# Performance work log

Measured on AMD Instinct MI355X. Metric: run time of the kernel, lower is better.

The kernel has to match this reference:

```python
import jax, jax.numpy as jnp
import numpy as np

B, L, H, HEADS = 4, 2048, 512, 8
D = H // HEADS  # 64


def setup_inputs() -> dict:
    key = jax.random.key(0)
    ks = jax.random.split(key, 13)
    s = 0.02
    return {
        "q_in": jax.random.normal(ks[0], (B, L, H), jnp.float32),
        "k_in": jax.random.normal(ks[1], (B, L, H), jnp.float32),
        "v_in": jax.random.normal(ks[2], (B, L, H), jnp.float32),
        "Wq_w": jax.random.normal(ks[3], (H, H), jnp.float32) * s,
        "Wq_b": jax.random.normal(ks[4], (H,), jnp.float32) * s,
        "Wk_w": jax.random.normal(ks[5], (H, H), jnp.float32) * s,
        "Wk_b": jax.random.normal(ks[6], (H,), jnp.float32) * s,
        "Wv_w": jax.random.normal(ks[7], (H, H), jnp.float32) * s,
        "Wv_b": jax.random.normal(ks[8], (H,), jnp.float32) * s,
        "Wo_w": jax.random.normal(ks[9], (H, H), jnp.float32) * s,
        "Wo_b": jax.random.normal(ks[10], (H,), jnp.float32) * s,
        "Wp_w": jax.random.normal(ks[11], (2 * L - 1, D), jnp.float32) * s,
        "Wp_b": jax.random.normal(ks[12], (2 * L - 1,), jnp.float32) * s,
    }


def _skew(p):
    # p: (b, h, l, 2l-1) -> relative-position bias (b, h, l, l) via pad/flatten/reshape skew trick
    b, h, l, _ = p.shape
    p = jnp.pad(p, ((0, 0), (0, 0), (0, 0), (0, 1)))          # (b,h,l,2l)
    p = p.reshape(b, h, 2 * l * l)
    p = jnp.pad(p, ((0, 0), (0, 0), (0, l - 1)))               # (b,h,(l+1)(2l-1))
    p = p.reshape(b, h, l + 1, 2 * l - 1)
    return p[:, :, :-1, -l:]                                   # (b,h,l,l)


def reference(q_in, k_in, v_in, Wq_w, Wq_b, Wk_w, Wk_b, Wv_w, Wv_b, Wo_w, Wo_b, Wp_w, Wp_b):
    b, l, hid = q_in.shape
    q = q_in @ Wq_w.T + Wq_b
    k = k_in @ Wk_w.T + Wk_b
    v = v_in @ Wv_w.T + Wv_b
    # (b, l, h*d) -> (b, h, l, d)
    to_heads = lambda x: x.reshape(b, l, HEADS, D).transpose(0, 2, 1, 3)
    q, k, v = to_heads(q), to_heads(k), to_heads(v)
    q = q / jnp.sqrt(jnp.asarray(D, q.dtype))  # scaling applied BEFORE posenc, as in original
    scores = jnp.einsum('bhid,bhjd->bhij', q, k)
    pos = _skew(q @ Wp_w.T + Wp_b)             # posenc linear applied to scaled q
    scores = scores + pos
    attn = jax.nn.softmax(scores, axis=-1)     # (b,h,l,l)
    # Original torch.einsum('b h l l, b h l d -> b h l d') takes the DIAGONAL of attn
    diag = jnp.diagonal(attn, axis1=-2, axis2=-1)  # (b,h,l)
    out = diag[..., None] * v                       # (b,h,l,d)
    out = out.transpose(0, 2, 1, 3).reshape(b, l, hid)
    return out @ Wo_w.T + Wo_b
```

## Files before the change

kernel.cpp:

```cpp
#include <hip/hip_runtime.h>
#include <cstdint>


typedef unsigned short u16;
typedef __bf16 bf16x8 __attribute__((ext_vector_type(8)));
typedef __bf16 bf16x2 __attribute__((ext_vector_type(2)));
typedef float  f32x16 __attribute__((ext_vector_type(16)));
typedef uint32_t __attribute__((address_space(1))) as1_u32;
typedef uint32_t __attribute__((address_space(3))) as3_u32;

__device__ __forceinline__ u16 f2bf(float f) {
  __bf16 h = (__bf16)f;
  return __builtin_bit_cast(u16, h);
}
__device__ __forceinline__ uint32_t pkbf(float a, float b) {
  bf16x2 v; v[0] = (__bf16)a; v[1] = (__bf16)b;
  return __builtin_bit_cast(uint32_t, v);
}
__device__ __forceinline__ float bf2f(u16 u) {
  return __uint_as_float(((uint32_t)u) << 16);
}
__device__ __forceinline__ float exp2v(float x) {
  float r;
  asm("v_exp_f32 %0, %1" : "=v"(r) : "v"(x));
  return r;
}
__device__ __forceinline__ void gl_lds16(const void* g, void* l) {
  __builtin_amdgcn_global_load_lds((const as1_u32*)g, (as3_u32*)l, 16, 0, 0);
}

__global__ __launch_bounds__(256) void prep_kernel(
    const float* __restrict__ qin, const float* __restrict__ kin, const float* __restrict__ vin,
    const float* __restrict__ wq,  const float* __restrict__ wk,  const float* __restrict__ wv,
    const float* __restrict__ wo,  const float* __restrict__ wp,
    u16* __restrict__ xq, u16* __restrict__ xk, u16* __restrict__ xv,
    u16* __restrict__ bwq, u16* __restrict__ bwk, u16* __restrict__ bwv,
    u16* __restrict__ bwo, u16* __restrict__ bwp) {
  long u = (long)blockIdx.x * 256 + threadIdx.x;
  const float* src; u16* dst; long off; float qs = 1.0f;
  if      (u < 524288L)  { src = qin; dst = xq;  off = u; }
  else if (u < 1048576L) { src = kin; dst = xk;  off = u - 524288L; }
  else if (u < 1572864L) { src = vin; dst = xv;  off = u - 1048576L; }
  else if (u < 1605632L) { src = wq;  dst = bwq; off = u - 1572864L; qs = 0.18033688f; }
  else if (u < 1638400L) { src = wk;  dst = bwk; off = u - 1605632L; }
  else if (u < 1671168L) { src = wv;  dst = bwv; off = u - 1638400L; }
  else if (u < 1703936L) { src = wo;  dst = bwo; off = u - 1671168L; }
  else if (u < 1736696L) { src = wp;  dst = bwp; off = u - 1703936L; }
  else {
    long o = (u - 1736696L) * 8 + 262080L;
    uint4 z = {0u, 0u, 0u, 0u};
    *(uint4*)(bwp + o) = z;
    return;
  }
  const float4* s4 = (const float4*)(src + off * 8);
  float4 a = s4[0], b = s4[1];
  uint32_t p0 = pkbf(a.x * qs, a.y * qs);
  uint32_t p1 = pkbf(a.z * qs, a.w * qs);
  uint32_t p2 = pkbf(b.x * qs, b.y * qs);
  uint32_t p3 = pkbf(b.z * qs, b.w * qs);
  uint4 o = {p0, p1, p2, p3};
  *(uint4*)(dst + off * 8) = o;
}

__device__ __forceinline__ void gemm64_core(
    const u16* __restrict__ A, const u16* __restrict__ W, int m0, int n0,
    u16* Al, u16* Bl, int tid, f32x16& acc) {
  const int lane = tid & 63, w = tid >> 6;
  const int wi = w >> 1, wj = w & 1;
  const int l31 = lane & 31, lh = lane >> 5;
  const int r = tid >> 2, ch = tid & 3;
  const int gch = ch ^ ((r >> 1) & 3);
  for (int kb = 0; kb < 16; ++kb) {
    gl_lds16(A + (long)(m0 + r) * 512 + kb * 32 + gch * 8, (char*)Al + w * 64 * 16);
    gl_lds16(W + (long)(n0 + r) * 512 + kb * 32 + gch * 8, (char*)Bl + w * 64 * 16);
    __syncthreads();
    bf16x8 af[2], bfr[2];
#pragma unroll
    for (int ks = 0; ks < 2; ++ks) {
      int c2 = 2 * ks + lh;
      int rA = 32 * wi + l31;
      int rB = 32 * wj + l31;
      af[ks]  = *(const bf16x8*)((char*)Al + (rA * 4 + (c2 ^ ((rA >> 1) & 3))) * 16);
      bfr[ks] = *(const bf16x8*)((char*)Bl + (rB * 4 + (c2 ^ ((rB >> 1) & 3))) * 16);
    }
#pragma unroll
    for (int ks = 0; ks < 2; ++ks)
      acc = __builtin_amdgcn_mfma_f32_32x32x16_bf16(af[ks], bfr[ks], acc, 0, 0, 0);
    __syncthreads();
  }
}

__global__ __launch_bounds__(256, 4) void gemm_bt(
    const u16* __restrict__ A, const u16* __restrict__ W, const float* __restrict__ bias,
    float* __restrict__ ofp) {
  __shared__ u16 Al[64 * 32];
  __shared__ u16 Bl[64 * 32];
  const int tid = threadIdx.x;
  const int lane = tid & 63, w = tid >> 6;
  const int wi = w >> 1, wj = w & 1;
  const int l31 = lane & 31, lh = lane >> 5;
  const int u = (blockIdx.x & 7) * 128 + (blockIdx.x >> 3);
  const int m0 = (u >> 3) * 64, n0 = (u & 7) * 64;

  float bv = bias[n0 + 32 * wj + l31];
  f32x16 acc;
#pragma unroll
  for (int rr = 0; rr < 16; ++rr) acc[rr] = bv;

  gemm64_core(A, W, m0, n0, Al, Bl, tid, acc);

  int n = n0 + 32 * wj + l31;
#pragma unroll
  for (int rr = 0; rr < 16; ++rr) {
    int row = m0 + 32 * wi + (rr & 3) + 8 * (rr >> 2) + 4 * lh;
    ofp[(long)row * 512 + n] = acc[rr];
  }
}

__global__ __launch_bounds__(256, 4) void qkv_gemm(
    const u16* __restrict__ xq, const u16* __restrict__ xk, const u16* __restrict__ xv,
    const u16* __restrict__ wqp, const u16* __restrict__ wkp, const u16* __restrict__ wvp,
    const float* __restrict__ bq, const float* __restrict__ bk, const float* __restrict__ bv,
    u16* __restrict__ oq, u16* __restrict__ ok, u16* __restrict__ ov) {
  __shared__ u16 Al[64 * 32];
  __shared__ u16 Bl[64 * 32];
  const int mat = blockIdx.x >> 10;
  const int t = blockIdx.x & 1023;
  const u16* A = (mat == 0) ? xq : (mat == 1) ? xk : xv;
  const u16* W = (mat == 0) ? wqp : (mat == 1) ? wkp : wvp;
  const float* bias = (mat == 0) ? bq : (mat == 1) ? bk : bv;
  u16* obf = (mat == 0) ? oq : (mat == 1) ? ok : ov;
  const float bsc = (mat == 0) ? 0.18033688f : 1.0f;

  const int tid = threadIdx.x;
  const int lane = tid & 63, w = tid >> 6;
  const int wi = w >> 1, wj = w & 1;
  const int l31 = lane & 31, lh = lane >> 5;
  const int u = (t & 7) * 128 + (t >> 3);
  const int m0 = (u >> 3) * 64, n0 = (u & 7) * 64;

  float bvv = bias[n0 + 32 * wj + l31] * bsc;
  f32x16 acc;
#pragma unroll
  for (int rr = 0; rr < 16; ++rr) acc[rr] = bvv;

  gemm64_core(A, W, m0, n0, Al, Bl, tid, acc);

  int n = n0 + 32 * wj + l31;
  int h = n >> 6, d = n & 63;
#pragma unroll
  for (int rr = 0; rr < 16; ++rr) {
    int row = m0 + 32 * wi + (rr & 3) + 8 * (rr >> 2) + 4 * lh;
    int b = row >> 11, l = row & 2047;
    obf[(((long)(b * 8 + h)) * 2048 + l) * 64 + d] = f2bf(acc[rr]);
  }
}

#define PCOMP(RING, G, AQ0, AQ1, AQ2, AQ3, B0, B1, B2, B3, BV)                   \
  do {                                                                           \
    f32x16 accP;                                                                 \
    _Pragma("unroll")                                                            \
    for (int r = 0; r < 16; ++r) accP[r] = (BV);                                 \
    accP = __builtin_amdgcn_mfma_f32_32x32x16_bf16(AQ0, B0, accP, 0, 0, 0);      \
    accP = __builtin_amdgcn_mfma_f32_32x32x16_bf16(AQ1, B1, accP, 0, 0, 0);      \
    accP = __builtin_amdgcn_mfma_f32_32x32x16_bf16(AQ2, B2, accP, 0, 0, 0);      \
    accP = __builtin_amdgcn_mfma_f32_32x32x16_bf16(AQ3, B3, accP, 0, 0, 0);      \
    int bw_ = 32 * (G) + l31 + 4 * lh;                                           \
    _Pragma("unroll")                                                            \
    for (int r = 0; r < 16; ++r) {                                               \
      const int lrr = (r & 3) + 8 * (r >> 2);                                    \
      int uu = (bw_ + lrr) & 127;                                                \
      (RING)[uu * 36 + lrr + 4 * lh] = f2bf(accP[r]);                            \
    }                                                                            \
  } while (0)

#define GATH(RING, T, ACC)                                                       \
  do {                                                                           \
    int u_ = (31 + l31 + 32 * (T)) & 127;                                        \
    const u16* p_ = (RING) + u_ * 36 + 4 * lh;                                   \
    uint2 g0 = *(const uint2*)(p_);                                              \
    uint2 g1 = *(const uint2*)(p_ + 8);                                          \
    uint2 g2 = *(const uint2*)(p_ + 16);                                         \
    uint2 g3 = *(const uint2*)(p_ + 24);                                         \
    ACC[0]  = __uint_as_float(g0.x << 16); ACC[1]  = __uint_as_float(g0.x & 0xffff0000u); \
    ACC[2]  = __uint_as_float(g0.y << 16); ACC[3]  = __uint_as_float(g0.y & 0xffff0000u); \
    ACC[4]  = __uint_as_float(g1.x << 16); ACC[5]  = __uint_as_float(g1.x & 0xffff0000u); \
    ACC[6]  = __uint_as_float(g1.y << 16); ACC[7]  = __uint_as_float(g1.y & 0xffff0000u); \
    ACC[8]  = __uint_as_float(g2.x << 16); ACC[9]  = __uint_as_float(g2.x & 0xffff0000u); \
    ACC[10] = __uint_as_float(g2.y << 16); ACC[11] = __uint_as_float(g2.y & 0xffff0000u); \
    ACC[12] = __uint_as_float(g3.x << 16); ACC[13] = __uint_as_float(g3.x & 0xffff0000u); \
    ACC[14] = __uint_as_float(g3.y << 16); ACC[15] = __uint_as_float(g3.y & 0xffff0000u); \
  } while (0)

#define ATTN_STEP(T, DO_P)                                                       \
  do {                                                                           \
    const int t_ = (T);                                                          \
    const u16* kp_ = kb + (long)(c0 + 32 * t_ + l31) * 64 + lh * 8;              \
    bf16x8 kf0 = *(const bf16x8*)(kp_);                                          \
    bf16x8 kf1 = *(const bf16x8*)(kp_ + 16);                                     \
    bf16x8 kf2 = *(const bf16x8*)(kp_ + 32);                                     \
    bf16x8 kf3 = *(const bf16x8*)(kp_ + 48);                                     \
    {                                                                            \
      f32x16 accS;                                                               \
      GATH(ringA, t_, accS);                                                     \
      accS = __builtin_amdgcn_mfma_f32_32x32x16_bf16(aqA0, kf0, accS, 0, 0, 0);  \
      accS = __builtin_amdgcn_mfma_f32_32x32x16_bf16(aqA1, kf1, accS, 0, 0, 0);  \
      accS = __builtin_amdgcn_mfma_f32_32x32x16_bf16(aqA2, kf2, accS, 0, 0, 0);  \
      accS = __builtin_amdgcn_mfma_f32_32x32x16_bf16(aqA3, kf3, accS, 0, 0, 0);  \
      if (diagw && t_ == tdA) {                                                  \
        _Pragma("unroll")                                                        \
        for (int r = 0; r < 16; ++r) {                                           \
          const int lrr = (r & 3) + 8 * (r >> 2);                                \
          if (l31 == lrr + 4 * lh) sdiag[lrr + 4 * lh] = accS[r];                \
        }                                                                        \
      }                                                                          \
      _Pragma("unroll")                                                          \
      for (int r = 0; r < 16; ++r) rsum[r] += exp2v(accS[r]);                    \
    }                                                                            \
    {                                                                            \
      f32x16 accS;                                                               \
      GATH(ringB, t_, accS);                                                     \
      accS = __builtin_amdgcn_mfma_f32_32x32x16_bf16(aqB0, kf0, accS, 0, 0, 0);  \
      accS = __builtin_amdgcn_mfma_f32_32x32x16_bf16(aqB1, kf1, accS, 0, 0, 0);  \
      accS = __builtin_amdgcn_mfma_f32_32x32x16_bf16(aqB2, kf2, accS, 0, 0, 0);  \
      accS = __builtin_amdgcn_mfma_f32_32x32x16_bf16(aqB3, kf3, accS, 0, 0, 0);  \
      if (diagw && t_ == tdA + 1) {                                              \
        _Pragma("unroll")                                                        \
        for (int r = 0; r < 16; ++r) {                                           \
          const int lrr = (r & 3) + 8 * (r >> 2);                                \
          if (l31 == lrr + 4 * lh) sdiag[32 + lrr + 4 * lh] = accS[r];           \
        }                                                                        \
      }                                                                          \
      _Pragma("unroll")                                                          \
      for (int r = 0; r < 16; ++r) rsum[16 + r] += exp2v(accS[r]);               \
    }                                                                            \
    if (DO_P) {                                                                  \
      int wr_ = wbA + 32 * (t_ + 2) + l31;                                       \
      const u16* bp_ = wpw + (long)wr_ * 64 + lh * 8;                            \
      bf16x8 nb0 = *(const bf16x8*)(bp_);                                        \
      bf16x8 nb1 = *(const bf16x8*)(bp_ + 16);                                   \
      bf16x8 nb2 = *(const bf16x8*)(bp_ + 32);                                   \
      bf16x8 nb3 = *(const bf16x8*)(bp_ + 48);                                   \
      float nbv = wpb[wr_ > 4094 ? 4094 : wr_] * 1.44269504f;                    \
      PCOMP(ringB, t_ + 2, aqB0, aqB1, aqB2, aqB3, cb0, cb1, cb2, cb3, cbv);     \
      PCOMP(ringA, t_ + 2, aqA0, aqA1, aqA2, aqA3, nb0, nb1, nb2, nb3, nbv);     \
      cb0 = nb0; cb1 = nb1; cb2 = nb2; cb3 = nb3; cbv = nbv;                     \
    }                                                                            \
  } while (0)

__global__ __launch_bounds__(256, 2) void attn_kernel(
    const u16* __restrict__ qw, const u16* __restrict__ kw, const u16* __restrict__ vw,
    const u16* __restrict__ wpw, const float* __restrict__ wpb, u16* __restrict__ outp) {
  __shared__ u16 Pl[8 * 128 * 36];
  __shared__ float sdiag[64];
  __shared__ float rssum[64 * 4];
  __shared__ float attw[64];

  const int tid = threadIdx.x, lane = tid & 63, w = tid >> 6;
  const int sbi = blockIdx.x;
  const int x = sbi & 7, g = sbi >> 3;
  const int bh = x + 8 * (g >> 5);
  const int it = g & 31;
  const int i0 = it * 64;
  const u16* qb = qw + (long)bh * 2048 * 64;
  const u16* kb = kw + (long)bh * 2048 * 64;
  const u16* vb = vw + (long)bh * 2048 * 64;

  const int l31 = lane & 31, lh = lane >> 5;
  const int c0 = w << 9;
  const int wbA = 2016 + c0 - i0;
  const bool diagw = (w == (it >> 3));
  const int tdA = 2 * (it & 7);

  u16* ringA = Pl + w * 9216;
  u16* ringB = ringA + 4608;

  bf16x8 aqA0, aqA1, aqA2, aqA3, aqB0, aqB1, aqB2, aqB3;
  {
    const u16* pA = qb + (long)(i0 + l31) * 64 + lh * 8;
    aqA0 = *(const bf16x8*)(pA);
    aqA1 = *(const bf16x8*)(pA + 16);
    aqA2 = *(const bf16x8*)(pA + 32);
    aqA3 = *(const bf16x8*)(pA + 48);
    const u16* pB = pA + 32 * 64;
    aqB0 = *(const bf16x8*)(pB);
    aqB1 = *(const bf16x8*)(pB + 16);
    aqB2 = *(const bf16x8*)(pB + 32);
    aqB3 = *(const bf16x8*)(pB + 48);
  }

  float rsum[32];
#pragma unroll
  for (int r = 0; r < 32; ++r) rsum[r] = 0.f;

  bf16x8 cb0, cb1, cb2, cb3;
  float cbv;

  {
    int wr = wbA - 32 + l31;
    const u16* bp = wpw + (long)wr * 64 + lh * 8;
    bf16x8 f0 = *(const bf16x8*)(bp), f1 = *(const bf16x8*)(bp + 16);
    bf16x8 f2 = *(const bf16x8*)(bp + 32), f3 = *(const bf16x8*)(bp + 48);
    float fv = wpb[wr > 4094 ? 4094 : wr] * 1.44269504f;
    PCOMP(ringB, 0, aqB0, aqB1, aqB2, aqB3, f0, f1, f2, f3, fv);
  }
  {
    int wr = wbA + l31;
    const u16* bp = wpw + (long)wr * 64 + lh * 8;
    bf16x8 f0 = *(const bf16x8*)(bp), f1 = *(const bf16x8*)(bp + 16);
    bf16x8 f2 = *(const bf16x8*)(bp + 32), f3 = *(const bf16x8*)(bp + 48);
    float fv = wpb[wr > 4094 ? 4094 : wr] * 1.44269504f;
    PCOMP(ringA, 0, aqA0, aqA1, aqA2, aqA3, f0, f1, f2, f3, fv);
    PCOMP(ringB, 1, aqB0, aqB1, aqB2, aqB3, f0, f1, f2, f3, fv);
  }
  {
    int wr = wbA + 32 + l31;
    const u16* bp = wpw + (long)wr * 64 + lh * 8;
    cb0 = *(const bf16x8*)(bp); cb1 = *(const bf16x8*)(bp + 16);
    cb2 = *(const bf16x8*)(bp + 32); cb3 = *(const bf16x8*)(bp + 48);
    cbv = wpb[wr > 4094 ? 4094 : wr] * 1.44269504f;
    PCOMP(ringA, 1, aqA0, aqA1, aqA2, aqA3, cb0, cb1, cb2, cb3, cbv);
  }

  for (int t = 0; t < 15; ++t) {
    ATTN_STEP(t, true);
  }
  ATTN_STEP(15, false);

#pragma unroll
  for (int r = 0; r < 32; ++r) {
    float v = rsum[r];
    v += __shfl_xor(v, 1);
    v += __shfl_xor(v, 2);
    v += __shfl_xor(v, 4);
    v += __shfl_xor(v, 8);
    v += __shfl_xor(v, 16);
    rsum[r] = v;
  }
  if (l31 == 0) {
#pragma unroll
    for (int r = 0; r < 16; ++r) {
      int lr = (r & 3) + 8 * (r >> 2) + 4 * lh;
      rssum[lr * 4 + w] = rsum[r];
      rssum[(32 + lr) * 4 + w] = rsum[16 + r];
    }
  }
  __syncthreads();
  if (tid < 64) {
    float S = rssum[tid * 4] + rssum[tid * 4 + 1] + rssum[tid * 4 + 2] + rssum[tid * 4 + 3];
    attw[tid] = exp2v(sdiag[tid]) / S;
  }
  __syncthreads();
  {
    int r = tid >> 2, dd = (tid & 3) * 16;
    float a = attw[r];
    int b = bh >> 3, h = bh & 7;
    const u16* vp = vb + (long)(i0 + r) * 64 + dd;
    u16* op = outp + ((long)(b * 2048 + i0 + r)) * 512 + h * 64 + dd;
    uint4 v0 = *(const uint4*)vp;
    uint4 v1 = *(const uint4*)(vp + 8);
    uint32_t vin[8] = {v0.x, v0.y, v0.z, v0.w, v1.x, v1.y, v1.z, v1.w};
    uint32_t vout[8];
#pragma unroll
    for (int e = 0; e < 8; ++e) {
      float lo = bf2f((u16)(vin[e] & 0xffffu)) * a;
      float hi = bf2f((u16)(vin[e] >> 16)) * a;
      vout[e] = pkbf(lo, hi);
    }
    uint4 o0 = {vout[0], vout[1], vout[2], vout[3]};
    uint4 o1 = {vout[4], vout[5], vout[6], vout[7]};
    *(uint4*)op = o0;
    *(uint4*)(op + 8) = o1;
  }
}

extern "C" void kernel_launch(void* const* d_in, const int* in_sizes, int n_in,
                              void* d_out, int out_size, void* d_ws, size_t ws_size,
                              hipStream_t stream) {
  (void)in_sizes; (void)n_in; (void)out_size; (void)ws_size;
  const float* q_in = (const float*)d_in[0];
  const float* k_in = (const float*)d_in[1];
  const float* v_in = (const float*)d_in[2];
  const float* Wq_w = (const float*)d_in[3];
  const float* Wq_b = (const float*)d_in[4];
  const float* Wk_w = (const float*)d_in[5];
  const float* Wk_b = (const float*)d_in[6];
  const float* Wv_w = (const float*)d_in[7];
  const float* Wv_b = (const float*)d_in[8];
  const float* Wo_w = (const float*)d_in[9];
  const float* Wo_b = (const float*)d_in[10];
  const float* Wp_w = (const float*)d_in[11];
  const float* Wp_b = (const float*)d_in[12];

  char* ws = (char*)d_ws;
  u16* xq    = (u16*)(ws + 0);
  u16* xk    = (u16*)(ws + 8388608);
  u16* xv    = (u16*)(ws + 16777216);
  u16* wq    = (u16*)(ws + 25165824);
  u16* wk    = (u16*)(ws + 25690112);
  u16* wv    = (u16*)(ws + 26214400);
  u16* wo    = (u16*)(ws + 26738688);
  u16* wp    = (u16*)(ws + 27262976);
  u16* q_ws  = (u16*)(ws + 27787264);
  u16* k_ws  = (u16*)(ws + 36175872);
  u16* v_ws  = (u16*)(ws + 44564480);
  u16* opre  = (u16*)(ws + 52953088);

  prep_kernel<<<6784, 256, 0, stream>>>(q_in, k_in, v_in, Wq_w, Wk_w, Wv_w, Wo_w, Wp_w,
                                        xq, xk, xv, wq, wk, wv, wo, wp);
  qkv_gemm<<<3072, 256, 0, stream>>>(xq, xk, xv, wq, wk, wv, Wq_b, Wk_b, Wv_b,
                                     q_ws, k_ws, v_ws);
  attn_kernel<<<1024, 256, 0, stream>>>(q_ws, k_ws, v_ws, wp, Wp_b, opre);
  gemm_bt<<<1024, 256, 0, stream>>>(opre, wo, Wo_b, (float*)d_out);
}
```

Baseline: 224.2 us.

## Software-pipeline K and posenc loads, prefetch ring gathers, and pad LDS rows

The attention loop now double-buffers K fragments and Wp rows in registers. The loads for step t+1 and t+2 are issued before the current step's MFMAs, and the next step's LDS gathers are done at the end of each step, so global and LDS latency overlap with compute. The LDS ring stride goes from 36 to 38 u16 per row and the gathers become 32-bit loads, which aims to reduce bank conflicts. The cost is higher register pressure under launch_bounds(256,2), which could cause spills, plus slightly more shared memory.

```diff
diff --git a/kernel.cpp b/kernel.cpp
--- a/kernel.cpp
+++ b/kernel.cpp
@@ -156,6 +156,26 @@
   }
 }
 
+#define LOADK(T, K0, K1, K2, K3)                                                 \
+  do {                                                                           \
+    const u16* kp_ = kb + (long)(c0 + 32 * (T) + l31) * 64 + lh * 8;             \
+    K0 = *(const bf16x8*)(kp_);                                                  \
+    K1 = *(const bf16x8*)(kp_ + 16);                                             \
+    K2 = *(const bf16x8*)(kp_ + 32);                                             \
+    K3 = *(const bf16x8*)(kp_ + 48);                                             \
+  } while (0)
+
+#define LOADNB(M, N0, N1, N2, N3, NV)                                            \
+  do {                                                                           \
+    int wr_ = wbA + 32 * (M) + l31;                                              \
+    const u16* bp_ = wpw + (long)wr_ * 64 + lh * 8;                              \
+    N0 = *(const bf16x8*)(bp_);                                                  \
+    N1 = *(const bf16x8*)(bp_ + 16);                                             \
+    N2 = *(const bf16x8*)(bp_ + 32);                                             \
+    N3 = *(const bf16x8*)(bp_ + 48);                                             \
+    NV = wpb[wr_ > 4094 ? 4094 : wr_] * 1.44269504f;                             \
+  } while (0)
+
 #define PCOMP(RING, G, AQ0, AQ1, AQ2, AQ3, B0, B1, B2, B3, BV)                   \
   do {                                                                           \
     f32x16 accP;                                                                 \
@@ -170,88 +190,71 @@
     for (int r = 0; r < 16; ++r) {                                               \
       const int lrr = (r & 3) + 8 * (r >> 2);                                    \
       int uu = (bw_ + lrr) & 127;                                                \
-      (RING)[uu * 36 + lrr + 4 * lh] = f2bf(accP[r]);                            \
+      (RING)[uu * 38 + lrr + 4 * lh] = f2bf(accP[r]);                            \
     }                                                                            \
   } while (0)
 
 #define GATH(RING, T, ACC)                                                       \
   do {                                                                           \
     int u_ = (31 + l31 + 32 * (T)) & 127;                                        \
-    const u16* p_ = (RING) + u_ * 36 + 4 * lh;                                   \
-    uint2 g0 = *(const uint2*)(p_);                                              \
-    uint2 g1 = *(const uint2*)(p_ + 8);                                          \
-    uint2 g2 = *(const uint2*)(p_ + 16);                                         \
-    uint2 g3 = *(const uint2*)(p_ + 24);                                         \
-    ACC[0]  = __uint_as_float(g0.x << 16); ACC[1]  = __uint_as_float(g0.x & 0xffff0000u); \
-    ACC[2]  = __uint_as_float(g0.y << 16); ACC[3]  = __uint_as_float(g0.y & 0xffff0000u); \
-    ACC[4]  = __uint_as_float(g1.x << 16); ACC[5]  = __uint_as_float(g1.x & 0xffff0000u); \
-    ACC[6]  = __uint_as_float(g1.y << 16); ACC[7]  = __uint_as_float(g1.y & 0xffff0000u); \
-    ACC[8]  = __uint_as_float(g2.x << 16); ACC[9]  = __uint_as_float(g2.x & 0xffff0000u); \
-    ACC[10] = __uint_as_float(g2.y << 16); ACC[11] = __uint_as_float(g2.y & 0xffff0000u); \
-    ACC[12] = __uint_as_float(g3.x << 16); ACC[13] = __uint_as_float(g3.x & 0xffff0000u); \
-    ACC[14] = __uint_as_float(g3.y << 16); ACC[15] = __uint_as_float(g3.y & 0xffff0000u); \
+    const uint32_t* p_ = (const uint32_t*)((RING) + u_ * 38 + 4 * lh);           \
+    uint32_t g0 = p_[0], g1 = p_[1], g2 = p_[4],  g3 = p_[5];                    \
+    uint32_t g4 = p_[8], g5 = p_[9], g6 = p_[12], g7 = p_[13];                   \
+    ACC[0]  = __uint_as_float(g0 << 16); ACC[1]  = __uint_as_float(g0 & 0xffff0000u); \
+    ACC[2]  = __uint_as_float(g1 << 16); ACC[3]  = __uint_as_float(g1 & 0xffff0000u); \
+    ACC[4]  = __uint_as_float(g2 << 16); ACC[5]  = __uint_as_float(g2 & 0xffff0000u); \
+    ACC[6]  = __uint_as_float(g3 << 16); ACC[7]  = __uint_as_float(g3 & 0xffff0000u); \
+    ACC[8]  = __uint_as_float(g4 << 16); ACC[9]  = __uint_as_float(g4 & 0xffff0000u); \
+    ACC[10] = __uint_as_float(g5 << 16); ACC[11] = __uint_as_float(g5 & 0xffff0000u); \
+    ACC[12] = __uint_as_float(g6 << 16); ACC[13] = __uint_as_float(g6 & 0xffff0000u); \
+    ACC[14] = __uint_as_float(g7 << 16); ACC[15] = __uint_as_float(g7 & 0xffff0000u); \
   } while (0)
 
-#define ATTN_STEP(T, DO_P)                                                       \
+#define ATTN_STEP(T, KC0, KC1, KC2, KC3, KN0, KN1, KN2, KN3,                     \
+                  NU0, NU1, NU2, NU3, NUV, NN0, NN1, NN2, NN3, NNV,              \
+                  DOK, DOP)                                                      \
   do {                                                                           \
     const int t_ = (T);                                                          \
-    const u16* kp_ = kb + (long)(c0 + 32 * t_ + l31) * 64 + lh * 8;              \
-    bf16x8 kf0 = *(const bf16x8*)(kp_);                                          \
-    bf16x8 kf1 = *(const bf16x8*)(kp_ + 16);                                     \
-    bf16x8 kf2 = *(const bf16x8*)(kp_ + 32);                                     \
-    bf16x8 kf3 = *(const bf16x8*)(kp_ + 48);                                     \
-    {                                                                            \
-      f32x16 accS;                                                               \
-      GATH(ringA, t_, accS);                                                     \
-      accS = __builtin_amdgcn_mfma_f32_32x32x16_bf16(aqA0, kf0, accS, 0, 0, 0);  \
-      accS = __builtin_amdgcn_mfma_f32_32x32x16_bf16(aqA1, kf1, accS, 0, 0, 0);  \
-      accS = __builtin_amdgcn_mfma_f32_32x32x16_bf16(aqA2, kf2, accS, 0, 0, 0);  \
-      accS = __builtin_amdgcn_mfma_f32_32x32x16_bf16(aqA3, kf3, accS, 0, 0, 0);  \
-      if (diagw && t_ == tdA) {                                                  \
-        _Pragma("unroll")                                                        \
-        for (int r = 0; r < 16; ++r) {                                           \
-          const int lrr = (r & 3) + 8 * (r >> 2);                                \
-          if (l31 == lrr + 4 * lh) sdiag[lrr + 4 * lh] = accS[r];                \
-        }                                                                        \
+    if (DOK) { LOADK(t_ + 1, KN0, KN1, KN2, KN3); }                              \
+    if (DOP) { LOADNB(t_ + 2, NN0, NN1, NN2, NN3, NNV); }                        \
+    accSA = __builtin_amdgcn_mfma_f32_32x32x16_bf16(aqA0, KC0, accSA, 0, 0, 0);  \
+    accSA = __builtin_amdgcn_mfma_f32_32x32x16_bf16(aqA1, KC1, accSA, 0, 0, 0);  \
+    accSA = __builtin_amdgcn_mfma_f32_32x32x16_bf16(aqA2, KC2, accSA, 0, 0, 0);  \
+    accSA = __builtin_amdgcn_mfma_f32_32x32x16_bf16(aqA3, KC3, accSA, 0, 0, 0);  \
+    accSB = __builtin_amdgcn_mfma_f32_32x32x16_bf16(aqB0, KC0, accSB, 0, 0, 0);  \
+    accSB = __builtin_amdgcn_mfma_f32_32x32x16_bf16(aqB1, KC1, accSB, 0, 0, 0);  \
+    accSB = __builtin_amdgcn_mfma_f32_32x32x16_bf16(aqB2, KC2, accSB, 0, 0, 0);  \
+    accSB = __builtin_amdgcn_mfma_f32_32x32x16_bf16(aqB3, KC3, accSB, 0, 0, 0);  \
+    if (diagw && t_ == tdA) {                                                    \
+      _Pragma("unroll")                                                          \
+      for (int r = 0; r < 16; ++r) {                                             \
+        const int lrr = (r & 3) + 8 * (r >> 2);                                  \
+        if (l31 == lrr + 4 * lh) sdiag[lrr + 4 * lh] = accSA[r];                 \
       }                                                                          \
+    }                                                                            \
+    if (diagw && t_ == tdA + 1) {                                                \
       _Pragma("unroll")                                                          \
-      for (int r = 0; r < 16; ++r) rsum[r] += exp2v(accS[r]);                    \
+      for (int r = 0; r < 16; ++r) {                                             \
+        const int lrr = (r & 3) + 8 * (r >> 2);                                  \
+        if (l31 == lrr + 4 * lh) sdiag[32 + lrr + 4 * lh] = accSB[r];            \
+      }                                                                          \
     }                                                                            \
-    {                                                                            \
-      f32x16 accS;                                                               \
-      GATH(ringB, t_, accS);                                                     \
-      accS = __builtin_amdgcn_mfma_f32_32x32x16_bf16(aqB0, kf0, accS, 0, 0, 0);  \
-      accS = __builtin_amdgcn_mfma_f32_32x32x16_bf16(aqB1, kf1, accS, 0, 0, 0);  \
-      accS = __builtin_amdgcn_mfma_f32_32x32x16_bf16(aqB2, kf2, accS, 0, 0, 0);  \
-      accS = __builtin_amdgcn_mfma_f32_32x32x16_bf16(aqB3, kf3, accS, 0, 0, 0);  \
-      if (diagw && t_ == tdA + 1) {                                              \
-        _Pragma("unroll")                                                        \
-        for (int r = 0; r < 16; ++r) {                                           \
-          const int lrr = (r & 3) + 8 * (r >> 2);                                \
-          if (l31 == lrr + 4 * lh) sdiag[32 + lrr + 4 * lh] = accS[r];           \
-        }                                                                        \
-      }                                                                          \
-      _Pragma("unroll")                                                          \
-      for (int r = 0; r < 16; ++r) rsum[16 + r] += exp2v(accS[r]);               \
-    }                                                                            \
-    if (DO_P) {                                                                  \
-      int wr_ = wbA + 32 * (t_ + 2) + l31;                                       \
-      const u16* bp_ = wpw + (long)wr_ * 64 + lh * 8;                            \
-      bf16x8 nb0 = *(const bf16x8*)(bp_);                                        \
-      bf16x8 nb1 = *(const bf16x8*)(bp_ + 16);                                   \
-      bf16x8 nb2 = *(const bf16x8*)(bp_ + 32);                                   \
-      bf16x8 nb3 = *(const bf16x8*)(bp_ + 48);                                   \
-      float nbv = wpb[wr_ > 4094 ? 4094 : wr_] * 1.44269504f;                    \
-      PCOMP(ringB, t_ + 2, aqB0, aqB1, aqB2, aqB3, cb0, cb1, cb2, cb3, cbv);     \
-      PCOMP(ringA, t_ + 2, aqA0, aqA1, aqA2, aqA3, nb0, nb1, nb2, nb3, nbv);     \
-      cb0 = nb0; cb1 = nb1; cb2 = nb2; cb3 = nb3; cbv = nbv;                     \
+    _Pragma("unroll")                                                            \
+    for (int r = 0; r < 16; ++r) rsum[r] += exp2v(accSA[r]);                     \
+    _Pragma("unroll")                                                            \
+    for (int r = 0; r < 16; ++r) rsum[16 + r] += exp2v(accSB[r]);                \
+    if (DOP) {                                                                   \
+      PCOMP(ringB, t_ + 2, aqB0, aqB1, aqB2, aqB3, NU0, NU1, NU2, NU3, NUV);     \
+      PCOMP(ringA, t_ + 2, aqA0, aqA1, aqA2, aqA3, NN0, NN1, NN2, NN3, NNV);     \
+      GATH(ringA, t_ + 1, accSA);                                                \
+      GATH(ringB, t_ + 1, accSB);                                                \
     }                                                                            \
   } while (0)
 
 __global__ __launch_bounds__(256, 2) void attn_kernel(
     const u16* __restrict__ qw, const u16* __restrict__ kw, const u16* __restrict__ vw,
     const u16* __restrict__ wpw, const float* __restrict__ wpb, u16* __restrict__ outp) {
-  __shared__ u16 Pl[8 * 128 * 36];
+  __shared__ u16 Pl[8 * 128 * 38];
   __shared__ float sdiag[64];
   __shared__ float rssum[64 * 4];
   __shared__ float attw[64];
@@ -272,8 +275,8 @@
   const bool diagw = (w == (it >> 3));
   const int tdA = 2 * (it & 7);
 
-  u16* ringA = Pl + w * 9216;
-  u16* ringB = ringA + 4608;
+  u16* ringA = Pl + w * 9728;
+  u16* ringB = ringA + 4864;
 
   bf16x8 aqA0, aqA1, aqA2, aqA3, aqB0, aqB1, aqB2, aqB3;
   {
@@ -293,39 +296,39 @@
 #pragma unroll
   for (int r = 0; r < 32; ++r) rsum[r] = 0.f;
 
-  bf16x8 cb0, cb1, cb2, cb3;
-  float cbv;
+  bf16x8 kfA0, kfA1, kfA2, kfA3, kfB0, kfB1, kfB2, kfB3;
+  bf16x8 nb00, nb01, nb02, nb03, nb10, nb11, nb12, nb13;
+  float nbv0, nbv1;
+  f32x16 accSA, accSB;
 
   {
-    int wr = wbA - 32 + l31;
-    const u16* bp = wpw + (long)wr * 64 + lh * 8;
-    bf16x8 f0 = *(const bf16x8*)(bp), f1 = *(const bf16x8*)(bp + 16);
-    bf16x8 f2 = *(const bf16x8*)(bp + 32), f3 = *(const bf16x8*)(bp + 48);
-    float fv = wpb[wr > 4094 ? 4094 : wr] * 1.44269504f;
-    PCOMP(ringB, 0, aqB0, aqB1, aqB2, aqB3, f0, f1, f2, f3, fv);
-  }
-  {
-    int wr = wbA + l31;
-    const u16* bp = wpw + (long)wr * 64 + lh * 8;
-    bf16x8 f0 = *(const bf16x8*)(bp), f1 = *(const bf16x8*)(bp + 16);
-    bf16x8 f2 = *(const bf16x8*)(bp + 32), f3 = *(const bf16x8*)(bp + 48);
-    float fv = wpb[wr > 4094 ? 4094 : wr] * 1.44269504f;
-    PCOMP(ringA, 0, aqA0, aqA1, aqA2, aqA3, f0, f1, f2, f3, fv);
-    PCOMP(ringB, 1, aqB0, aqB1, aqB2, aqB3, f0, f1, f2, f3, fv);
-  }
-  {
-    int wr = wbA + 32 + l31;
-    const u16* bp = wpw + (long)wr * 64 + lh * 8;
-    cb0 = *(const bf16x8*)(bp); cb1 = *(const bf16x8*)(bp + 16);
-    cb2 = *(const bf16x8*)(bp + 32); cb3 = *(const bf16x8*)(bp + 48);
-    cbv = wpb[wr > 4094 ? 4094 : wr] * 1.44269504f;
-    PCOMP(ringA, 1, aqA0, aqA1, aqA2, aqA3, cb0, cb1, cb2, cb3, cbv);
-  }
-
-  for (int t = 0; t < 15; ++t) {
-    ATTN_STEP(t, true);
-  }
-  ATTN_STEP(15, false);
+    bf16x8 t0, t1, t2, t3; float tv;
+    LOADNB(-1, t0, t1, t2, t3, tv);
+    PCOMP(ringB, 0, aqB0, aqB1, aqB2, aqB3, t0, t1, t2, t3, tv);
+    LOADNB(0, t0, t1, t2, t3, tv);
+    PCOMP(ringA, 0, aqA0, aqA1, aqA2, aqA3, t0, t1, t2, t3, tv);
+    PCOMP(ringB, 1, aqB0, aqB1, aqB2, aqB3, t0, t1, t2, t3, tv);
+    LOADNB(1, nb10, nb11, nb12, nb13, nbv1);
+    PCOMP(ringA, 1, aqA0, aqA1, aqA2, aqA3, nb10, nb11, nb12, nb13, nbv1);
+    LOADK(0, kfA0, kfA1, kfA2, kfA3);
+    GATH(ringA, 0, accSA);
+    GATH(ringB, 0, accSB);
+  }
+
+  for (int tt = 0; tt < 14; tt += 2) {
+    ATTN_STEP(tt,     kfA0, kfA1, kfA2, kfA3, kfB0, kfB1, kfB2, kfB3,
+              nb10, nb11, nb12, nb13, nbv1, nb00, nb01, nb02, nb03, nbv0,
+              true, true);
+    ATTN_STEP(tt + 1, kfB0, kfB1, kfB2, kfB3, kfA0, kfA1, kfA2, kfA3,
+              nb00, nb01, nb02, nb03, nbv0, nb10, nb11, nb12, nb13, nbv1,
+              true, true);
+  }
+  ATTN_STEP(14, kfA0, kfA1, kfA2, kfA3, kfB0, kfB1, kfB2, kfB3,
+            nb10, nb11, nb12, nb13, nbv1, nb00, nb01, nb02, nb03, nbv0,
+            true, true);
+  ATTN_STEP(15, kfB0, kfB1, kfB2, kfB3, kfA0, kfA1, kfA2, kfA3,
+            nb00, nb01, nb02, nb03, nbv0, nb10, nb11, nb12, nb13, nbv1,
+            false, false);
 
 #pragma unroll
   for (int r = 0; r < 32; ++r) {
```

Result: slower. 229.6 us (+2.4%).
